# Kernel optimization log

Measured on AMD Instinct MI355X. Metric: run time of the kernel, lower is better.

## Reference

```python
import jax, jax.numpy as jnp
import numpy as np

DIM = 8          # per-head dim
ATT_EPS = 1e-15
BN_EPS = 1e-6


def setup_inputs() -> dict:
    key = jax.random.key(0)
    ks = jax.random.split(key, 6)
    B, C, H, W = 8, 256, 64, 64
    td = 256                      # heads * dim = 32 * 8
    return {
        'x':      jax.random.normal(ks[0], (B, C, H, W), jnp.float32),
        'w_qkv':  jax.random.normal(ks[1], (3 * td, C), jnp.float32) * 0.05,
        'w_dw':   jax.random.normal(ks[2], (3 * td, 1, 5, 5), jnp.float32) * 0.05,
        'w_pw':   jax.random.normal(ks[3], (96, 8, 8), jnp.float32) * 0.05,   # (groups, out/g, in/g)
        'w_proj': jax.random.normal(ks[4], (C, 2 * td), jnp.float32) * 0.05,
        'bn_gamma': jnp.ones((C,), jnp.float32),
        'bn_beta':  jnp.zeros((C,), jnp.float32),
        'bn_mean':  jnp.zeros((C,), jnp.float32),
        'bn_var':   jnp.ones((C,), jnp.float32),
    }


def _relu_linear_att(ms, H, W):
    # ms: [B, C, H, W] with C = heads * 3*DIM
    B = ms.shape[0]
    d = DIM
    qkv = ms.reshape(B, -1, 3 * d, H * W).transpose(0, 1, 3, 2)   # [B, h, N, 3d]
    q = jax.nn.relu(qkv[..., :d])
    k = jax.nn.relu(qkv[..., d:2 * d])
    v = qkv[..., 2 * d:]
    v = jnp.pad(v, ((0, 0), (0, 0), (0, 0), (0, 1)), constant_values=1.0)  # ones column
    kv = jnp.einsum('bhnd,bhne->bhde', k, v)                       # [B, h, d, d+1]
    out = jnp.einsum('bhnd,bhde->bhne', q, kv)                     # [B, h, N, d+1]
    out = out[..., :-1] / (out[..., -1:] + ATT_EPS)
    return out.transpose(0, 1, 3, 2).reshape(B, -1, H, W)          # [B, h*d, H, W]


def reference(x, w_qkv, w_dw, w_pw, w_proj, bn_gamma, bn_beta, bn_mean, bn_var):
    B, C, H, W = x.shape
    # 1x1 qkv projection
    qkv = jnp.einsum('oc,bchw->bohw', w_qkv, x)                    # [B, 768, H, W]
    # multiscale aggregation: 5x5 depthwise then grouped 1x1 (groups = 3*heads = 96)
    dw = jax.lax.conv_general_dilated(
        qkv, w_dw, window_strides=(1, 1), padding=[(2, 2), (2, 2)],
        dimension_numbers=('NCHW', 'OIHW', 'NCHW'),
        feature_group_count=qkv.shape[1])
    G, O, I = w_pw.shape
    agg = jnp.einsum('goi,bgihw->bgohw', w_pw,
                     dw.reshape(B, G, I, H, W)).reshape(B, G * O, H, W)
    ms = jnp.concatenate([qkv, agg], axis=1)                       # [B, 1536, H, W]
    att = _relu_linear_att(ms, H, W)                               # [B, 512, H, W]
    # proj: 1x1 conv + BatchNorm (eval mode) + identity activation
    p = jnp.einsum('oc,bchw->bohw', w_proj, att)                   # [B, 256, H, W]
    inv = bn_gamma / jnp.sqrt(bn_var + BN_EPS)
    p = p * inv[None, :, None, None] + (bn_beta - bn_mean * inv)[None, :, None, None]
    return x + p
```

## Files before the change

### kernel.cpp

```cpp
#include <hip/hip_runtime.h>
#include <hip/hip_bf16.h>


#define HW 4096
#define ATT_EPS 1e-15f
#define BN_EPS 1e-6f

typedef __attribute__((ext_vector_type(8))) short short8;
typedef __attribute__((ext_vector_type(4))) short short4v;
typedef __attribute__((ext_vector_type(4))) float f32x4;
typedef __attribute__((ext_vector_type(2))) float f32x2;
typedef __attribute__((ext_vector_type(8))) unsigned short u16x8;
typedef __attribute__((ext_vector_type(4))) unsigned short u16x4;

static __device__ inline short f2bf(float f) {
    union { float f; unsigned u; } v; v.f = f;
    unsigned r = v.u + 0x7fff + ((v.u >> 16) & 1);
    return (short)(r >> 16);
}
static __device__ inline float bf2f(unsigned short u) {
    union { unsigned u; float f; } v; v.u = (unsigned)u << 16; return v.f;
}

__global__ __launch_bounds__(256) void prep_w(const float* __restrict__ wproj,
                                              unsigned short* __restrict__ wbf) {
    const int i = (blockIdx.x * 256 + threadIdx.x) * 4;
    float4 v = *(const float4*)&wproj[i];
    u16x4 r = {(unsigned short)f2bf(v.x), (unsigned short)f2bf(v.y),
               (unsigned short)f2bf(v.z), (unsigned short)f2bf(v.w)};
    *(u16x4*)&wbf[i] = r;
}

__global__ __launch_bounds__(256) void prep_wq(const float* __restrict__ wqkv,
                                               unsigned short* __restrict__ wqbf) {
    const int i = (blockIdx.x * 256 + threadIdx.x) * 4;
    float4 v = *(const float4*)&wqkv[i];
    u16x4 r = {(unsigned short)f2bf(v.x), (unsigned short)f2bf(v.y),
               (unsigned short)f2bf(v.z), (unsigned short)f2bf(v.w)};
    *(u16x4*)&wqbf[i] = r;
}

__global__ __launch_bounds__(256) void qkv_gemm(const float* __restrict__ x,
                                                const unsigned short* __restrict__ wqbf,
                                                unsigned short* __restrict__ qkv) {
    __shared__ unsigned short B_l[128 * 40];
    const int t  = threadIdx.x;
    const int b  = blockIdx.z;
    const int ob = blockIdx.y * 128;
    const int nb = blockIdx.x * 128;

    const int lane = t & 63, wave = t >> 6;
    const int wo = (wave >> 1) * 64, wn = (wave & 1) * 64;
    const int am = lane & 15, ak = lane >> 4;

    const unsigned short* ap0 = wqbf + (size_t)(ob + wo + am) * 256 + ak * 8;

    const int n   = t & 127;
    const int kg0 = t >> 7;
    const float* xb = x + (size_t)b * 256 * HW + nb + n;

    f32x4 acc[4][4];
#pragma unroll
    for (int s = 0; s < 4; s++)
#pragma unroll
        for (int u = 0; u < 4; u++) acc[s][u] = (f32x4){0.f, 0.f, 0.f, 0.f};

    for (int kb = 0; kb < 256; kb += 32) {
        short8 af[4];
#pragma unroll
        for (int s = 0; s < 4; s++)
            af[s] = *(const short8*)(ap0 + (size_t)s * 16 * 256 + kb);

        __syncthreads();
#pragma unroll
        for (int q = 0; q < 2; q++) {
            const int kg = kg0 + q * 2;
            u16x8 pk;
#pragma unroll
            for (int j = 0; j < 8; j++) {
                float v = xb[(size_t)(kb + kg * 8 + j) * HW];
                pk[j] = (unsigned short)f2bf(v);
            }
            *(u16x8*)&B_l[n * 40 + kg * 8] = pk;
        }
        __syncthreads();

        short8 bf[4];
#pragma unroll
        for (int u = 0; u < 4; u++)
            bf[u] = *(const short8*)&B_l[(wn + u * 16 + am) * 40 + ak * 8];
#pragma unroll
        for (int s = 0; s < 4; s++)
#pragma unroll
            for (int u = 0; u < 4; u++)
                acc[s][u] = __builtin_amdgcn_mfma_f32_16x16x32_bf16(af[s], bf[u], acc[s][u], 0, 0, 0);
    }

#pragma unroll
    for (int s = 0; s < 4; s++)
#pragma unroll
        for (int u = 0; u < 4; u++)
#pragma unroll
            for (int r = 0; r < 4; r++) {
                const int o = ob + wo + s * 16 + (lane >> 4) * 4 + r;
                const int nn = nb + wn + u * 16 + (lane & 15);
                qkv[((size_t)b * 768 + o) * HW + nn] = (unsigned short)f2bf(acc[s][u][r]);
            }
}

__global__ __launch_bounds__(256, 6) void dw_agg(const unsigned short* __restrict__ qkv,
                                                 const float* __restrict__ wdw,
                                                 const float* __restrict__ wpw,
                                                 unsigned short* __restrict__ agg) {
    __shared__ float tile_raw[8 + 4 * 20 * 64 + 8];
    float* tile = tile_raw + 8;
    const int b = blockIdx.z, g = blockIdx.y;
    const int y0 = blockIdx.x * 16;
    const int t = threadIdx.x;
    const int tx = t & 15, ty = t >> 4;

    const float* wkg = wdw + g * 8 * 25;
    const float* pwg = wpw + g * 64;

    float out[8][4];
#pragma unroll
    for (int o = 0; o < 8; o++)
#pragma unroll
        for (int j = 0; j < 4; j++) out[o][j] = 0.f;

#pragma unroll 1
    for (int half = 0; half < 2; half++) {
        if (half) __syncthreads();
#pragma unroll
        for (int k = 0; k < 3; k++) {
            const int i = t + 256 * k;
            if (i < 640) {
                const int c8 = i & 7, rr = (i >> 3) % 20, ch = i / 160;
                const int y = y0 - 2 + rr;
                u16x8 v = {0, 0, 0, 0, 0, 0, 0, 0};
                if (y >= 0 && y < 64)
                    v = *(const u16x8*)&qkv[((size_t)(b * 768 + g * 8 + half * 4 + ch)) * HW + y * 64 + c8 * 8];
                f32x4 lo = {bf2f(v[0]), bf2f(v[1]), bf2f(v[2]), bf2f(v[3])};
                f32x4 hi = {bf2f(v[4]), bf2f(v[5]), bf2f(v[6]), bf2f(v[7])};
                *(f32x4*)&tile[i * 8]     = lo;
                *(f32x4*)&tile[i * 8 + 4] = hi;
            }
        }
        __syncthreads();

#pragma unroll 1
        for (int ch4 = 0; ch4 < 4; ch4++) {
            const int ch = half * 4 + ch4;
            const float* wkc = wkg + ch * 25;
            float a0 = 0.f, a1 = 0.f, a2 = 0.f, a3 = 0.f;
#pragma unroll
            for (int dy = 0; dy < 5; dy++) {
                const int off = ch4 * 1280 + (ty + dy) * 64 + tx * 4;
                f32x4 C = *(const f32x4*)&tile[off];
                f32x2 L = *(const f32x2*)&tile[off - 2];
                f32x2 R = *(const f32x2*)&tile[off + 4];
                float win[8];
                win[0] = (tx == 0)  ? 0.f : L[0];
                win[1] = (tx == 0)  ? 0.f : L[1];
                win[2] = C[0]; win[3] = C[1];
                win[4] = C[2]; win[5] = C[3];
                win[6] = (tx == 15) ? 0.f : R[0];
                win[7] = (tx == 15) ? 0.f : R[1];
#pragma unroll
                for (int dx = 0; dx < 5; dx++) {
                    const float wv = wkc[dy * 5 + dx];
                    a0 += wv * win[dx + 0];
                    a1 += wv * win[dx + 1];
                    a2 += wv * win[dx + 2];
                    a3 += wv * win[dx + 3];
                }
            }
#pragma unroll
            for (int o = 0; o < 8; o++) {
                const float wv = pwg[o * 8 + ch];
                out[o][0] += wv * a0; out[o][1] += wv * a1;
                out[o][2] += wv * a2; out[o][3] += wv * a3;
            }
        }
    }

#pragma unroll
    for (int o = 0; o < 8; o++) {
        u16x4 rv = {(unsigned short)f2bf(out[o][0]), (unsigned short)f2bf(out[o][1]),
                    (unsigned short)f2bf(out[o][2]), (unsigned short)f2bf(out[o][3])};
        *(u16x4*)&agg[((size_t)(b * 768 + g * 8 + o)) * HW + (y0 + ty) * 64 + tx * 4] = rv;
    }
}

__global__ __launch_bounds__(256) void kv_pass(const unsigned short* __restrict__ qkv,
                                               const unsigned short* __restrict__ agg,
                                               float* __restrict__ kvpart) {
    const int t = threadIdx.x;
    const int w = t >> 6, lane = t & 63;
    const int hp = blockIdx.x * 4 + w;
    const int b = blockIdx.y, c = blockIdx.z;
    const int h0 = hp * 2, h1 = h0 + 1;
    const unsigned short* buf = (h0 < 32) ? qkv : agg;
    const int cb0 = (h0 & 31) * 24, cb1 = (h1 & 31) * 24;

    const int row = lane & 15, kgrp = lane >> 4;
    const int n0 = c * 256 + kgrp * 8;

    const int chA = (row < 8) ? (cb0 + 8 + row) : (cb1 + row);
    const unsigned short* ap = buf + ((size_t)b * 768 + chA) * HW + n0;

    const bool bload = (row < 8);
    const unsigned short* bp0 = buf + ((size_t)b * 768 + cb0 + 16 + (row & 7)) * HW + n0;
    const unsigned short* bp1 = buf + ((size_t)b * 768 + cb1 + 16 + (row & 7)) * HW + n0;
    const short cfill = (row == 8) ? (short)0x3F80 : (short)0;
    const short8 bconst = {cfill, cfill, cfill, cfill, cfill, cfill, cfill, cfill};

    f32x4 acc0 = {0.f, 0.f, 0.f, 0.f};
    f32x4 acc1 = {0.f, 0.f, 0.f, 0.f};

#pragma unroll
    for (int i = 0; i < 8; i++) {
        u16x8 av = *(const u16x8*)(ap + i * 32);
        short8 b0 = bload ? *(const short8*)(bp0 + i * 32) : bconst;
        short8 b1 = bload ? *(const short8*)(bp1 + i * 32) : bconst;
        short8 ar;
#pragma unroll
        for (int j = 0; j < 8; j++)
            ar[j] = (short)((av[j] & 0x8000) ? 0 : av[j]);
        acc0 = __builtin_amdgcn_mfma_f32_16x16x32_bf16(ar, b0, acc0, 0, 0, 0);
        acc1 = __builtin_amdgcn_mfma_f32_16x16x32_bf16(ar, b1, acc1, 0, 0, 0);
    }

    if (row <= 8) {
        float* kp;
        f32x4 a;
        int dbase;
        if (kgrp < 2) {
            kp = kvpart + (size_t)c * 36864 + (size_t)(b * 64 + h0) * 72;
            a = acc0; dbase = kgrp * 4;
        } else {
            kp = kvpart + (size_t)c * 36864 + (size_t)(b * 64 + h1) * 72;
            a = acc1; dbase = (kgrp - 2) * 4;
        }
#pragma unroll
        for (int r = 0; r < 4; r++)
            kp[(dbase + r) * 9 + row] = a[r];
    }
}

__global__ __launch_bounds__(256) void kv_red(const float* __restrict__ kvpart,
                                              float* __restrict__ kvout) {
    const int i = blockIdx.x * 256 + threadIdx.x;
    float s = 0.f;
#pragma unroll
    for (int c = 0; c < 16; c++) s += kvpart[(size_t)c * 36864 + i];
    kvout[i] = s;
}

__global__ __launch_bounds__(256) void att_pass(const unsigned short* __restrict__ qkv,
                                                const unsigned short* __restrict__ agg,
                                                const float* __restrict__ kvbuf,
                                                unsigned short* __restrict__ att_f) {
    const int h = blockIdx.y, b = blockIdx.z;
    const int t = threadIdx.x;
    const float* kvp = kvbuf + ((size_t)(b * 64 + h)) * 72;

    float kvr[72];
#pragma unroll
    for (int i = 0; i < 18; i++) {
        f32x4 v = *(const f32x4*)&kvp[i * 4];
        kvr[i * 4 + 0] = v[0]; kvr[i * 4 + 1] = v[1];
        kvr[i * 4 + 2] = v[2]; kvr[i * 4 + 3] = v[3];
    }

    const unsigned short* buf = (h < 32) ? qkv : agg;
    const int cbase = (h & 31) * 24;
    const int n0 = (blockIdx.x * 256 + t) * 8;
    const unsigned short* qp = buf + ((size_t)b * 768 + cbase) * HW + n0;

    float q[8][8];
#pragma unroll
    for (int d = 0; d < 8; d++) {
        u16x8 v = *(const u16x8*)&qp[(size_t)d * HW];
#pragma unroll
        for (int j = 0; j < 8; j++) q[d][j] = fmaxf(bf2f(v[j]), 0.f);
    }

    unsigned short* op = att_f + (((size_t)(b * 64 + h)) * HW + n0) * 8;
#pragma unroll
    for (int j = 0; j < 8; j++) {
        float num[9];
#pragma unroll
        for (int e = 0; e < 9; e++) num[e] = 0.f;
#pragma unroll
        for (int d = 0; d < 8; d++) {
            const float qv = q[d][j];
#pragma unroll
            for (int e = 0; e < 9; e++) num[e] += qv * kvr[d * 9 + e];
        }
        const float rden = 1.f / (num[8] + ATT_EPS);
        u16x8 r;
#pragma unroll
        for (int e = 0; e < 8; e++) r[e] = (unsigned short)f2bf(num[e] * rden);
        *(u16x8*)&op[j * 8] = r;
    }
}

__global__ __launch_bounds__(256) void proj_gemm(const unsigned short* __restrict__ wbf,
                                                 const unsigned short* __restrict__ att_f,
                                                 const float* __restrict__ gamma,
                                                 const float* __restrict__ beta,
                                                 const float* __restrict__ mean,
                                                 const float* __restrict__ var,
                                                 const float* __restrict__ x,
                                                 float* __restrict__ out) {
    const int t  = threadIdx.x;
    const int b  = blockIdx.z;
    const int ob = blockIdx.y * 128;
    const int nb = blockIdx.x * 128;
    const int lane = t & 63, wave = t >> 6;
    const int wo = (wave >> 1) * 64, wn = (wave & 1) * 64;

    const int am = lane & 15, ak = lane >> 4;
    const unsigned short* ap0 = wbf + (size_t)(ob + wo + am) * 512 + ak * 8;
    const unsigned short* bp0 = att_f +
        (((size_t)b * 64 + ak) * HW + nb + wn + am) * 8;

    f32x4 acc[4][4];
#pragma unroll
    for (int s = 0; s < 4; s++)
#pragma unroll
        for (int u = 0; u < 4; u++) acc[s][u] = (f32x4){0.f, 0.f, 0.f, 0.f};

    for (int kb = 0; kb < 512; kb += 32) {
        short8 af[4], bf[4];
#pragma unroll
        for (int s = 0; s < 4; s++)
            af[s] = *(const short8*)(ap0 + (size_t)s * 16 * 512 + kb);
#pragma unroll
        for (int u = 0; u < 4; u++)
            bf[u] = *(const short8*)(bp0 + ((size_t)(kb >> 3) * HW + u * 16) * 8);
#pragma unroll
        for (int s = 0; s < 4; s++)
#pragma unroll
            for (int u = 0; u < 4; u++)
                acc[s][u] = __builtin_amdgcn_mfma_f32_16x16x32_bf16(af[s], bf[u], acc[s][u], 0, 0, 0);
    }

#pragma unroll
    for (int s = 0; s < 4; s++) {
        const int o_base = ob + wo + s * 16 + (lane >> 4) * 4;
#pragma unroll
        for (int r = 0; r < 4; r++) {
            const int o = o_base + r;
            const float inv = gamma[o] * rsqrtf(var[o] + BN_EPS);
            const float sh  = beta[o] - mean[o] * inv;
#pragma unroll
            for (int u = 0; u < 4; u++) {
                const int n = nb + wn + u * 16 + (lane & 15);
                const size_t idx = ((size_t)b * 256 + o) * HW + n;
                out[idx] = x[idx] + acc[s][u][r] * inv + sh;
            }
        }
    }
}

extern "C" void kernel_launch(void* const* d_in, const int* in_sizes, int n_in,
                              void* d_out, int out_size, void* d_ws, size_t ws_size,
                              hipStream_t stream) {
    const float* x      = (const float*)d_in[0];
    const float* w_qkv  = (const float*)d_in[1];
    const float* w_dw   = (const float*)d_in[2];
    const float* w_pw   = (const float*)d_in[3];
    const float* w_proj = (const float*)d_in[4];
    const float* gamma  = (const float*)d_in[5];
    const float* beta   = (const float*)d_in[6];
    const float* mean   = (const float*)d_in[7];
    const float* var    = (const float*)d_in[8];
    float* out = (float*)d_out;

    unsigned short* qkv  = (unsigned short*)d_ws;
    unsigned short* agg  = qkv + (size_t)25165824;
    unsigned short* attf = agg + (size_t)25165824;
    unsigned short* wbf  = attf + (size_t)16777216;
    float* kvb = (float*)(wbf + (size_t)131072);
    float* kvpart = (float*)attf;
    unsigned short* wqbf = attf + (size_t)4194304;

    prep_w  <<<dim3(128),       256, 0, stream>>>(w_proj, wbf);
    prep_wq <<<dim3(192),       256, 0, stream>>>(w_qkv, wqbf);
    qkv_gemm<<<dim3(32, 6, 8),  256, 0, stream>>>(x, wqbf, qkv);
    dw_agg  <<<dim3(4, 96, 8),  256, 0, stream>>>(qkv, w_dw, w_pw, agg);
    kv_pass <<<dim3(8, 8, 16),  256, 0, stream>>>(qkv, agg, kvpart);
    kv_red  <<<dim3(144),       256, 0, stream>>>(kvpart, kvb);
    att_pass<<<dim3(2, 64, 8),  256, 0, stream>>>(qkv, agg, kvb, attf);
    proj_gemm<<<dim3(32, 2, 8), 256, 0, stream>>>(wbf, attf,
                                                  gamma, beta, mean, var, x, out);
}
```

Before: 227.3 us.

## Pre-transpose x to bf16 N-major layout and drop LDS staging in qkv GEMM

Adds a prep kernel that converts x to bf16 and transposes it to [B, N, C] through shared memory, writing into the agg buffer, which is not yet in use at that point. The qkv GEMM then loads B fragments directly from global memory as contiguous 16-byte vectors, with no LDS staging and no per-iteration barriers. Previously each of the 6 output-row blocks re-read strided fp32 x and converted it again. The cost is an extra kernel launch and an extra write and read of a 16 MB bf16 copy of x.

```diff
diff --git a/kernel.cpp b/kernel.cpp
--- a/kernel.cpp
+++ b/kernel.cpp
@@ -40,24 +40,45 @@
     *(u16x4*)&wqbf[i] = r;
 }
 
-__global__ __launch_bounds__(256) void qkv_gemm(const float* __restrict__ x,
+__global__ __launch_bounds__(256) void prep_xt(const float* __restrict__ x,
+                                               unsigned short* __restrict__ xt) {
+    __shared__ unsigned short tl[64][72];
+    const int b = blockIdx.z;
+    const int c0 = blockIdx.y * 64, n0 = blockIdx.x * 64;
+    const int t = threadIdx.x;
+    const int nq = t & 15, cl = t >> 4;
+#pragma unroll
+    for (int p = 0; p < 4; p++) {
+        const int c = cl + p * 16;
+        float4 v = *(const float4*)&x[((size_t)b * 256 + c0 + c) * HW + n0 + nq * 4];
+        tl[nq * 4 + 0][c] = (unsigned short)f2bf(v.x);
+        tl[nq * 4 + 1][c] = (unsigned short)f2bf(v.y);
+        tl[nq * 4 + 2][c] = (unsigned short)f2bf(v.z);
+        tl[nq * 4 + 3][c] = (unsigned short)f2bf(v.w);
+    }
+    __syncthreads();
+#pragma unroll
+    for (int k = 0; k < 2; k++) {
+        const int slot = t + 256 * k;
+        const int nl = slot >> 3, oct = slot & 7;
+        u16x8 v = *(const u16x8*)&tl[nl][oct * 8];
+        *(u16x8*)&xt[((size_t)b * 4096 + n0 + nl) * 256 + c0 + oct * 8] = v;
+    }
+}
+
+__global__ __launch_bounds__(256) void qkv_gemm(const unsigned short* __restrict__ xt,
                                                 const unsigned short* __restrict__ wqbf,
                                                 unsigned short* __restrict__ qkv) {
-    __shared__ unsigned short B_l[128 * 40];
     const int t  = threadIdx.x;
     const int b  = blockIdx.z;
     const int ob = blockIdx.y * 128;
     const int nb = blockIdx.x * 128;
-
     const int lane = t & 63, wave = t >> 6;
     const int wo = (wave >> 1) * 64, wn = (wave & 1) * 64;
     const int am = lane & 15, ak = lane >> 4;
 
     const unsigned short* ap0 = wqbf + (size_t)(ob + wo + am) * 256 + ak * 8;
-
-    const int n   = t & 127;
-    const int kg0 = t >> 7;
-    const float* xb = x + (size_t)b * 256 * HW + nb + n;
+    const unsigned short* bp0 = xt + ((size_t)b * 4096 + nb + wn + am) * 256 + ak * 8;
 
     f32x4 acc[4][4];
 #pragma unroll
@@ -66,29 +87,13 @@
         for (int u = 0; u < 4; u++) acc[s][u] = (f32x4){0.f, 0.f, 0.f, 0.f};
 
     for (int kb = 0; kb < 256; kb += 32) {
-        short8 af[4];
+        short8 af[4], bf[4];
 #pragma unroll
         for (int s = 0; s < 4; s++)
             af[s] = *(const short8*)(ap0 + (size_t)s * 16 * 256 + kb);
-
-        __syncthreads();
-#pragma unroll
-        for (int q = 0; q < 2; q++) {
-            const int kg = kg0 + q * 2;
-            u16x8 pk;
-#pragma unroll
-            for (int j = 0; j < 8; j++) {
-                float v = xb[(size_t)(kb + kg * 8 + j) * HW];
-                pk[j] = (unsigned short)f2bf(v);
-            }
-            *(u16x8*)&B_l[n * 40 + kg * 8] = pk;
-        }
-        __syncthreads();
-
-        short8 bf[4];
 #pragma unroll
         for (int u = 0; u < 4; u++)
-            bf[u] = *(const short8*)&B_l[(wn + u * 16 + am) * 40 + ak * 8];
+            bf[u] = *(const short8*)(bp0 + (size_t)u * 16 * 256 + kb);
 #pragma unroll
         for (int s = 0; s < 4; s++)
 #pragma unroll
@@ -386,10 +391,12 @@
     float* kvb = (float*)(wbf + (size_t)131072);
     float* kvpart = (float*)attf;
     unsigned short* wqbf = attf + (size_t)4194304;
+    unsigned short* xt   = agg;
 
     prep_w  <<<dim3(128),       256, 0, stream>>>(w_proj, wbf);
     prep_wq <<<dim3(192),       256, 0, stream>>>(w_qkv, wqbf);
-    qkv_gemm<<<dim3(32, 6, 8),  256, 0, stream>>>(x, wqbf, qkv);
+    prep_xt <<<dim3(64, 4, 8),  256, 0, stream>>>(x, xt);
+    qkv_gemm<<<dim3(32, 6, 8),  256, 0, stream>>>(xt, wqbf, qkv);
     dw_agg  <<<dim3(4, 96, 8),  256, 0, stream>>>(qkv, w_dw, w_pw, agg);
     kv_pass <<<dim3(8, 8, 16),  256, 0, stream>>>(qkv, agg, kvpart);
     kv_red  <<<dim3(144),       256, 0, stream>>>(kvpart, kvb);
```

Result: slower. 249.1 us (+9.6%).
